# Kernel optimization log

Hardware: AMD Instinct MI355X
Metric: run time of the kernel (lower is better)

## Reference

```python
import jax, jax.numpy as jnp
import numpy as np

B, N, L, H = 8, 64, 256, 768
E = 2 * H            # 1536, concat(subj, obj)
NH = 12              # attention heads
HD = E // NH         # 128 head dim
HL = 1024            # LSTM hidden
C = 42               # num classes
SCALE = 0.02         # param scale for numerical sanity


def setup_inputs() -> dict:
    key = jax.random.key(0)
    ks = jax.random.split(key, 19)
    rn = lambda k, s: jax.random.normal(k, s, jnp.float32) * SCALE
    return {
        "hidden": jax.random.normal(ks[0], (B, N, L, H), jnp.float32),
        "entity_pair_inds": jax.random.randint(ks[1], (B, N, 2), 0, L),
        "Wkey": jax.random.uniform(ks[2], (E, E), jnp.float32) * SCALE,
        "Wque": jax.random.uniform(ks[3], (E, E), jnp.float32) * SCALE,
        "Wval": jax.random.uniform(ks[4], (E, E), jnp.float32) * SCALE,
        "in_proj_w": rn(ks[5], (3 * E, E)),
        "in_proj_b": rn(ks[6], (3 * E,)),
        "out_proj_w": rn(ks[7], (E, E)),
        "out_proj_b": rn(ks[8], (E,)),
        "Wih_f": rn(ks[9], (4 * HL, E)),
        "Whh_f": rn(ks[10], (4 * HL, HL)),
        "bih_f": rn(ks[11], (4 * HL,)),
        "bhh_f": rn(ks[12], (4 * HL,)),
        "Wih_b": rn(ks[13], (4 * HL, E)),
        "Whh_b": rn(ks[14], (4 * HL, HL)),
        "bih_b": rn(ks[15], (4 * HL,)),
        "bhh_b": rn(ks[16], (4 * HL,)),
        "out_w": rn(ks[17], (C, 2 * HL)),
        "out_b": rn(ks[18], (C,)),
    }


def _mha(q_in, k_in, v_in, in_proj_w, in_proj_b, out_proj_w, out_proj_b):
    # torch nn.MultiheadAttention, batch_first
    Wq, Wk, Wv = jnp.split(in_proj_w, 3, axis=0)
    bq, bk, bv = jnp.split(in_proj_b, 3, axis=0)
    b, n, _ = q_in.shape
    q = (q_in @ Wq.T + bq).reshape(b, n, NH, HD)
    k = (k_in @ Wk.T + bk).reshape(b, n, NH, HD)
    v = (v_in @ Wv.T + bv).reshape(b, n, NH, HD)
    scores = jnp.einsum("bnhd,bmhd->bhnm", q, k) / np.sqrt(HD).astype(np.float32)
    attn = jax.nn.softmax(scores, axis=-1)
    o = jnp.einsum("bhnm,bmhd->bnhd", attn, v).reshape(b, n, E)
    return o @ out_proj_w.T + out_proj_b


def _lstm_dir(x, Wih, Whh, bih, bhh):
    # single-direction LSTM over an unbatched sequence x: (T, E)
    def step(carry, xt):
        h, c = carry
        g = xt @ Wih.T + bih + h @ Whh.T + bhh  # (4*HL,)
        i, f, gg, o = jnp.split(g, 4)
        i, f, o = jax.nn.sigmoid(i), jax.nn.sigmoid(f), jax.nn.sigmoid(o)
        c = f * c + i * jnp.tanh(gg)
        h = o * jnp.tanh(c)
        return (h, c), h
    init = (jnp.zeros(HL, x.dtype), jnp.zeros(HL, x.dtype))
    _, hs = jax.lax.scan(step, init, x)
    return hs  # (T, HL)


def reference(hidden, entity_pair_inds, Wkey, Wque, Wval, in_proj_w, in_proj_b,
              out_proj_w, out_proj_b, Wih_f, Whh_f, bih_f, bhh_f,
              Wih_b, Whh_b, bih_b, bhh_b, out_w, out_b):
    # vectorized entity-pair gather: (B, N, 2) indices into token axis L
    idx = entity_pair_inds[:, :, :, None]                      # (B,N,2,1)
    pair = jnp.take_along_axis(hidden, idx, axis=2)            # (B,N,2,H)
    cat = pair.reshape(B, N, 2 * H)                            # (B,N,1536) = [subj; obj]
    keys = cat @ Wkey
    queries = cat @ Wque
    values = cat @ Wval
    # original calls attn(keys, queries, values) -> query=keys, key=queries, value=values
    attn_out = _mha(keys, queries, values, in_proj_w, in_proj_b, out_proj_w, out_proj_b)
    avg = jnp.sum(attn_out * cat, axis=1) / N                  # (B, E)
    # dropout is identity in eval mode
    # torch LSTM treats 2D input as unbatched sequence of length B
    hf = _lstm_dir(avg, Wih_f, Whh_f, bih_f, bhh_f)            # (B, HL)
    hb = _lstm_dir(avg[::-1], Wih_b, Whh_b, bih_b, bhh_b)[::-1]
    lstm_out = jnp.concatenate([hf, hb], axis=-1)              # (B, 2*HL)
    logits = lstm_out @ out_w.T + out_b                        # (B, C)
    return jax.nn.softmax(logits, axis=1)
```

## Files before the change

kernel.cpp:

```cpp
#include <hip/hip_runtime.h>
#include <hip/hip_bf16.h>
#include <cstdint>


typedef __attribute__((ext_vector_type(8))) short short8_t;
typedef __attribute__((ext_vector_type(4))) float f32x4_t;

__device__ __forceinline__ uint4 pack8(float4 a, float4 b) {
  union { uint4 u; __hip_bfloat16 h[8]; } pk;
  pk.h[0] = __float2bfloat16(a.x); pk.h[1] = __float2bfloat16(a.y);
  pk.h[2] = __float2bfloat16(a.z); pk.h[3] = __float2bfloat16(a.w);
  pk.h[4] = __float2bfloat16(b.x); pk.h[5] = __float2bfloat16(b.y);
  pk.h[6] = __float2bfloat16(b.z); pk.h[7] = __float2bfloat16(b.w);
  return pk.u;
}

__global__ __launch_bounds__(256) void prep_all_kernel(
    const float* __restrict__ hidden, const int* __restrict__ inds,
    const float* __restrict__ Wkey, const float* __restrict__ Wque, const float* __restrict__ Wval,
    const float* __restrict__ Whh_f, const float* __restrict__ Whh_b,
    float* __restrict__ cat, __hip_bfloat16* __restrict__ cat16,
    __hip_bfloat16* __restrict__ Wt16, __hip_bfloat16* __restrict__ whh16s,
    float* __restrict__ avg0) {
  const int bid = blockIdx.x, tid = threadIdx.x;
  if (bid < 512) {
    if (bid < 48) avg0[bid * 256 + tid] = 0.f;
    int bn = bid;
    int i0 = inds[bn * 2 + 0], i1 = inds[bn * 2 + 1];
    const float* r0 = hidden + ((size_t)bn * 256 + i0) * 768;
    const float* r1 = hidden + ((size_t)bn * 256 + i1) * 768;
    float* c = cat + (size_t)bn * 1536;
    __hip_bfloat16* c16 = cat16 + (size_t)bn * 1536;
    for (int i = tid; i < 768; i += 256) {
      float a = r0[i], b = r1[i];
      c[i] = a; c[768 + i] = b;
      c16[i] = __float2bfloat16(a); c16[768 + i] = __float2bfloat16(b);
    }
  } else if (bid < 7424) {
    int b2 = bid - 512;
    int z = b2 / 2304, rem = b2 % 2304, by = rem / 48, bx = rem % 48;
    const float* W = z == 0 ? Wkey : (z == 1 ? Wque : Wval);
    __hip_bfloat16* O = Wt16 + (size_t)z * 1536 * 1536;
    __shared__ float tile[32][33];
    int n0 = bx * 32, k0 = by * 32;
    int r = tid >> 3, c4 = (tid & 7) * 4;
    float4 v = *(const float4*)(W + (size_t)(k0 + r) * 1536 + n0 + c4);
    tile[r][c4] = v.x; tile[r][c4 + 1] = v.y; tile[r][c4 + 2] = v.z; tile[r][c4 + 3] = v.w;
    __syncthreads();
    union { ushort4 u; __hip_bfloat16 h[4]; } pk;
#pragma unroll
    for (int j = 0; j < 4; ++j) pk.h[j] = __float2bfloat16(tile[c4 + j][r]);
    *(ushort4*)(O + (size_t)(n0 + r) * 1536 + k0 + c4) = pk.u;
  } else {
    int id = (bid - 7424) * 256 + tid;
    int lane = id & 63, half = (id >> 6) & 1, row = (id >> 7) & 4095, d = id >> 19;
    const float* W = d ? Whh_b : Whh_f;
    const float* srcp = W + (size_t)row * 1024 + half * 512 + lane;
    union { uint4 u; __hip_bfloat16 h[8]; } pk;
#pragma unroll
    for (int e = 0; e < 8; ++e) pk.h[e] = __float2bfloat16(srcp[e * 64]);
    *(uint4*)(whh16s + (size_t)id * 8) = pk.u;
  }
}

template <int CMODE, bool BIAS, bool BF32B>
__global__ __launch_bounds__(256) void mfma_gemm(
    const __hip_bfloat16* __restrict__ A, long As,
    const void* __restrict__ Bmv, long Bs,
    const float* __restrict__ bias, long biasS,
    void* __restrict__ Cp, long Cs,
    const float* __restrict__ catp, float* __restrict__ avgp) {
  constexpr int K = 1536, N = 1536;
  const int z = blockIdx.z;
  A += (size_t)z * As;
  if (BIAS) bias += (size_t)z * biasS;
  __shared__ __align__(16) short Abuf[64 * 64];
  __shared__ __align__(16) short Bbuf[64 * 64];
  const int t = threadIdx.x;
  const int i0 = blockIdx.y * 64, j0 = blockIdx.x * 64;
  const int row = t >> 2, kq = t & 3;
  const int lane = t & 63, wave = t >> 6, wr = wave >> 1, wc = wave & 1;
  f32x4_t acc[2][2] = {};

  const char* Ag = (const char*)(A + (size_t)(i0 + row) * K) + kq * 32;
  const char* Bg;
  if (BF32B)
    Bg = (const char*)((const float*)Bmv + (size_t)z * Bs + (size_t)(j0 + row) * K) + kq * 64;
  else
    Bg = (const char*)((const __hip_bfloat16*)Bmv + (size_t)z * Bs + (size_t)(j0 + row) * K) + kq * 32;
  const int swz = (row & 7) << 4;
  char* Asw0 = (char*)Abuf + ((row * 128 + kq * 32) ^ swz);
  char* Asw1 = (char*)Abuf + ((row * 128 + kq * 32 + 16) ^ swz);
  char* Bsw0 = (char*)Bbuf + ((row * 128 + kq * 32) ^ swz);
  char* Bsw1 = (char*)Bbuf + ((row * 128 + kq * 32 + 16) ^ swz);

  for (int kb = 0; kb < K * 2; kb += 128) {
    uint4 a0 = *(const uint4*)(Ag + kb);
    uint4 a1 = *(const uint4*)(Ag + kb + 16);
    uint4 b0, b1;
    if (BF32B) {
      const char* p = Bg + kb * 2;
      float4 f0 = *(const float4*)(p);
      float4 f1 = *(const float4*)(p + 16);
      float4 f2 = *(const float4*)(p + 32);
      float4 f3 = *(const float4*)(p + 48);
      b0 = pack8(f0, f1); b1 = pack8(f2, f3);
    } else {
      b0 = *(const uint4*)(Bg + kb);
      b1 = *(const uint4*)(Bg + kb + 16);
    }
    __syncthreads();
    *(uint4*)Asw0 = a0; *(uint4*)Asw1 = a1;
    *(uint4*)Bsw0 = b0; *(uint4*)Bsw1 = b1;
    __syncthreads();
#pragma unroll
    for (int ks = 0; ks < 2; ++ks) {
      short8_t af[2], bfr[2];
#pragma unroll
      for (int mi = 0; mi < 2; ++mi) {
        int rr = wr * 32 + mi * 16 + (lane & 15);
        int off = (rr * 128 + ks * 64 + (lane >> 4) * 16) ^ ((rr & 7) << 4);
        af[mi] = *(const short8_t*)((const char*)Abuf + off);
      }
#pragma unroll
      for (int ni = 0; ni < 2; ++ni) {
        int rr = wc * 32 + ni * 16 + (lane & 15);
        int off = (rr * 128 + ks * 64 + (lane >> 4) * 16) ^ ((rr & 7) << 4);
        bfr[ni] = *(const short8_t*)((const char*)Bbuf + off);
      }
#pragma unroll
      for (int mi = 0; mi < 2; ++mi)
#pragma unroll
        for (int ni = 0; ni < 2; ++ni)
          acc[mi][ni] = __builtin_amdgcn_mfma_f32_16x16x32_bf16(af[mi], bfr[ni], acc[mi][ni], 0, 0, 0);
    }
  }
  if (CMODE == 2) {
#pragma unroll
    for (int ni = 0; ni < 2; ++ni) {
      int col = j0 + wc * 32 + ni * 16 + (lane & 15);
      float bv = bias[col];
      float p = 0.f;
#pragma unroll
      for (int mi = 0; mi < 2; ++mi) {
        int rbase = i0 + wr * 32 + mi * 16 + (lane >> 4) * 4;
#pragma unroll
        for (int r = 0; r < 4; ++r) {
          float val = acc[mi][ni][r] + bv;
          p += val * catp[(size_t)(rbase + r) * 1536 + col];
        }
      }
      p += __shfl_xor(p, 16);
      p += __shfl_xor(p, 32);
      if (lane < 16) atomicAdd(&avgp[(size_t)blockIdx.y * 1536 + col], p * (1.0f / 64.0f));
    }
  } else {
#pragma unroll
    for (int mi = 0; mi < 2; ++mi)
#pragma unroll
      for (int ni = 0; ni < 2; ++ni) {
        int r0 = i0 + wr * 32 + mi * 16 + (lane >> 4) * 4;
        int col = j0 + wc * 32 + ni * 16 + (lane & 15);
        float bv = BIAS ? bias[col] : 0.f;
#pragma unroll
        for (int r = 0; r < 4; ++r) {
          float val = acc[mi][ni][r] + bv;
          if (CMODE == 1)
            ((__hip_bfloat16*)Cp)[(size_t)z * Cs + (size_t)(r0 + r) * N + col] = __float2bfloat16(val);
          else
            ((float*)Cp)[(size_t)z * Cs + (size_t)(r0 + r) * N + col] = val;
        }
      }
  }
}

__global__ __launch_bounds__(256) void attn2_kernel(
    const __hip_bfloat16* __restrict__ qkv, __hip_bfloat16* __restrict__ o) {
  __shared__ __align__(16) ushort Qs[64 * 128];
  __shared__ __align__(16) ushort Ks[64 * 128];
  __shared__ __align__(16) ushort Vt[128 * 72];
  __shared__ __align__(16) ushort Ps[64 * 72];
  __shared__ float redmax[2][64];
  __shared__ float redsum[2][64];
  const int b = blockIdx.x / 12, h = blockIdx.x % 12;
  const int tid = threadIdx.x, lane = tid & 63, wave = tid >> 6;
  const int wr = wave >> 1, wc = wave & 1;
  const size_t base = (size_t)b * 64 * 1536 + (size_t)h * 128;
  const __hip_bfloat16* qg = qkv + base;
  const __hip_bfloat16* kg = qkv + 786432 + base;
  const __hip_bfloat16* vg = qkv + 2 * 786432 + base;

  for (int s = tid; s < 1024; s += 256) {
    int row = s >> 4, q4 = s & 15;
    int q4s = (q4 & 8) | ((q4 & 7) ^ (row & 7));
    uint4 qv = *(const uint4*)(qg + (size_t)row * 1536 + q4 * 8);
    uint4 kv = *(const uint4*)(kg + (size_t)row * 1536 + q4 * 8);
    *(uint4*)&Qs[row * 128 + q4s * 8] = qv;
    *(uint4*)&Ks[row * 128 + q4s * 8] = kv;
    uint4 vv = *(const uint4*)(vg + (size_t)row * 1536 + q4 * 8);
    const ushort* ve = (const ushort*)&vv;
    int colv = (((row >> 3) ^ (q4 & 7)) << 3) | (row & 7);
#pragma unroll
    for (int e = 0; e < 8; ++e) Vt[(q4 * 8 + e) * 72 + colv] = ve[e];
  }
  __syncthreads();

  f32x4_t sacc[2][2] = {};
#pragma unroll
  for (int ks = 0; ks < 4; ++ks) {
    short8_t qf[2], kf[2];
#pragma unroll
    for (int mi = 0; mi < 2; ++mi) {
      int rr = wr * 32 + mi * 16 + (lane & 15);
      int slot = ks * 4 + (lane >> 4);
      int slot2 = (slot & 8) | ((slot & 7) ^ (rr & 7));
      qf[mi] = *(const short8_t*)&Qs[rr * 128 + slot2 * 8];
    }
#pragma unroll
    for (int ni = 0; ni < 2; ++ni) {
      int rr = wc * 32 + ni * 16 + (lane & 15);
      int slot = ks * 4 + (lane >> 4);
      int slot2 = (slot & 8) | ((slot & 7) ^ (rr & 7));
      kf[ni] = *(const short8_t*)&Ks[rr * 128 + slot2 * 8];
    }
#pragma unroll
    for (int mi = 0; mi < 2; ++mi)
#pragma unroll
      for (int ni = 0; ni < 2; ++ni)
        sacc[mi][ni] = __builtin_amdgcn_mfma_f32_16x16x32_bf16(qf[mi], kf[ni], sacc[mi][ni], 0, 0, 0);
  }

  const float scale = 0.08838834764831845f;
  float pv[2][2][4];
#pragma unroll
  for (int mi = 0; mi < 2; ++mi)
#pragma unroll
    for (int r = 0; r < 4; ++r) {
      float a0 = sacc[mi][0][r] * scale, a1 = sacc[mi][1][r] * scale;
      pv[mi][0][r] = a0; pv[mi][1][r] = a1;
      float m0 = fmaxf(a0, a1);
      m0 = fmaxf(m0, __shfl_xor(m0, 1));
      m0 = fmaxf(m0, __shfl_xor(m0, 2));
      m0 = fmaxf(m0, __shfl_xor(m0, 4));
      m0 = fmaxf(m0, __shfl_xor(m0, 8));
      if ((lane & 15) == 0) redmax[wc][wr * 32 + mi * 16 + (lane >> 4) * 4 + r] = m0;
    }
  __syncthreads();
#pragma unroll
  for (int mi = 0; mi < 2; ++mi)
#pragma unroll
    for (int r = 0; r < 4; ++r) {
      int row = wr * 32 + mi * 16 + (lane >> 4) * 4 + r;
      float gm = fmaxf(redmax[0][row], redmax[1][row]);
      float e0 = __expf(pv[mi][0][r] - gm);
      float e1 = __expf(pv[mi][1][r] - gm);
      pv[mi][0][r] = e0; pv[mi][1][r] = e1;
      float s0 = e0 + e1;
      s0 += __shfl_xor(s0, 1);
      s0 += __shfl_xor(s0, 2);
      s0 += __shfl_xor(s0, 4);
      s0 += __shfl_xor(s0, 8);
      if ((lane & 15) == 0) redsum[wc][row] = s0;
      int col0 = wc * 32 + (lane & 15);
      Ps[row * 72 + col0] = __bfloat16_as_ushort(__float2bfloat16(e0));
      Ps[row * 72 + col0 + 16] = __bfloat16_as_ushort(__float2bfloat16(e1));
    }
  __syncthreads();

  f32x4_t oacc[2][4] = {};
#pragma unroll
  for (int ks = 0; ks < 2; ++ks) {
    short8_t pf[2], vf[4];
#pragma unroll
    for (int mi = 0; mi < 2; ++mi) {
      int rr = wr * 32 + mi * 16 + (lane & 15);
      pf[mi] = *(const short8_t*)&Ps[rr * 72 + ks * 32 + (lane >> 4) * 8];
    }
#pragma unroll
    for (int ni = 0; ni < 4; ++ni) {
      int rr = wc * 64 + ni * 16 + (lane & 15);
      int mb = (ks * 4 + (lane >> 4)) ^ ((rr >> 3) & 7);
      vf[ni] = *(const short8_t*)&Vt[rr * 72 + mb * 8];
    }
#pragma unroll
    for (int mi = 0; mi < 2; ++mi)
#pragma unroll
      for (int ni = 0; ni < 4; ++ni)
        oacc[mi][ni] = __builtin_amdgcn_mfma_f32_16x16x32_bf16(pf[mi], vf[ni], oacc[mi][ni], 0, 0, 0);
  }

#pragma unroll
  for (int mi = 0; mi < 2; ++mi)
#pragma unroll
    for (int r = 0; r < 4; ++r) {
      int row = wr * 32 + mi * 16 + (lane >> 4) * 4 + r;
      float inv = 1.f / (redsum[0][row] + redsum[1][row]);
#pragma unroll
      for (int ni = 0; ni < 4; ++ni) {
        int col = wc * 64 + ni * 16 + (lane & 15);
        o[base + (size_t)row * 1536 + col] = __float2bfloat16(oacc[mi][ni][r] * inv);
      }
    }
}

__global__ __launch_bounds__(256) void lstm_pre2_kernel(
    const float* __restrict__ avg,
    const float* __restrict__ Wih_f, const float* __restrict__ bih_f, const float* __restrict__ bhh_f,
    const float* __restrict__ Wih_b, const float* __restrict__ bih_b, const float* __restrict__ bhh_b,
    float* __restrict__ xg) {
  int g = blockIdx.x * 4 + (threadIdx.x >> 6);
  int lane = threadIdx.x & 63;
  int d = g >> 12, j = g & 4095;
  const float* W = d ? Wih_b : Wih_f;
  const float4* wrow = (const float4*)(W + (size_t)j * 1536);
  float4 w[6];
#pragma unroll
  for (int c = 0; c < 6; ++c) w[c] = wrow[c * 64 + lane];
  float s[8] = {};
#pragma unroll
  for (int r = 0; r < 8; ++r) {
    const float4* av = (const float4*)(avg + (size_t)r * 1536);
#pragma unroll
    for (int c = 0; c < 6; ++c) {
      float4 x = av[c * 64 + lane];
      s[r] += w[c].x * x.x + w[c].y * x.y + w[c].z * x.z + w[c].w * x.w;
    }
  }
#pragma unroll
  for (int r = 0; r < 8; ++r)
#pragma unroll
    for (int off = 32; off; off >>= 1) s[r] += __shfl_xor(s[r], off);
  if (lane == 0) {
    float bias = d ? (bih_b[j] + bhh_b[j]) : (bih_f[j] + bhh_f[j]);
#pragma unroll
    for (int r = 0; r < 8; ++r) xg[((size_t)d * 8 + r) * 4096 + j] = s[r] + bias;
  }
}

__global__ __launch_bounds__(256) void lstm_step2_kernel(
    const __hip_bfloat16* __restrict__ whh16s, const float* __restrict__ xg,
    float* __restrict__ hstate, float* __restrict__ cstate,
    float* __restrict__ hout, int s) {
  const int bid = blockIdx.x;
  const int d = bid >> 8, u0 = (bid & 255) * 4;
  const int tid = threadIdx.x, wave = tid >> 6, lane = tid & 63;
  const float* hread = hstate + ((size_t)(s & 1) * 2 + d) * 1024;
  float* hwrite = hstate + ((size_t)((s + 1) & 1) * 2 + d) * 1024;
  float* c = cstate + (size_t)d * 1024;
  const int r = d ? (7 - s) : s;

  float hreg[16];
  if (s == 0) {
#pragma unroll
    for (int cc = 0; cc < 16; ++cc) hreg[cc] = 0.f;
  } else {
#pragma unroll
    for (int cc = 0; cc < 16; ++cc) hreg[cc] = hread[cc * 64 + lane];
  }

  __shared__ float gsm[4][4];
#pragma unroll
  for (int ui = 0; ui < 4; ++ui) {
    int row = wave * 1024 + u0 + ui;
    const uint4* wp = (const uint4*)whh16s + ((size_t)d * 4096 + row) * 128 + lane;
    uint4 w0 = wp[0];
    uint4 w1 = wp[64];
    float sacc = 0.f;
#pragma unroll
    for (int e4 = 0; e4 < 4; ++e4) {
      uint32_t u = ((const uint32_t*)&w0)[e4];
      sacc += __uint_as_float(u << 16) * hreg[2 * e4] +
              __uint_as_float(u & 0xffff0000u) * hreg[2 * e4 + 1];
    }
#pragma unroll
    for (int e4 = 0; e4 < 4; ++e4) {
      uint32_t u = ((const uint32_t*)&w1)[e4];
      sacc += __uint_as_float(u << 16) * hreg[8 + 2 * e4] +
              __uint_as_float(u & 0xffff0000u) * hreg[8 + 2 * e4 + 1];
    }
#pragma unroll
    for (int off = 32; off; off >>= 1) sacc += __shfl_xor(sacc, off);
    if (lane == 0) gsm[wave][ui] = sacc;
  }
  __syncthreads();
  if (tid < 4) {
    int u = u0 + tid;
    const float* xgr = xg + ((size_t)d * 8 + r) * 4096;
    float gi = gsm[0][tid] + xgr[u];
    float gf = gsm[1][tid] + xgr[1024 + u];
    float gg = gsm[2][tid] + xgr[2048 + u];
    float go = gsm[3][tid] + xgr[3072 + u];
    float iv = 1.f / (1.f + __expf(-gi));
    float fv = 1.f / (1.f + __expf(-gf));
    float ov = 1.f / (1.f + __expf(-go));
    float cold = (s == 0) ? 0.f : c[u];
    float cn = fv * cold + iv * tanhf(gg);
    float hn = ov * tanhf(cn);
    c[u] = cn;
    hwrite[u] = hn;
    hout[((size_t)d * 8 + r) * 1024 + u] = hn;
  }
}

__global__ __launch_bounds__(256) void final_kernel(
    const float* __restrict__ hout, const float* __restrict__ out_w,
    const float* __restrict__ out_b, float* __restrict__ outp) {
  __shared__ float lo[2048];
  __shared__ float logits[64];
  const int s = blockIdx.x, tid = threadIdx.x;
  for (int i = tid; i < 1024; i += 256) {
    lo[i] = hout[(size_t)s * 1024 + i];
    lo[1024 + i] = hout[(size_t)(8 + s) * 1024 + i];
  }
  __syncthreads();
  const int wave = tid >> 6, lane = tid & 63;
  for (int cls = wave; cls < 42; cls += 4) {
    const float4* wr = (const float4*)(out_w + (size_t)cls * 2048);
    const float4* xr = (const float4*)lo;
    float acc = 0.f;
#pragma unroll
    for (int t = 0; t < 8; ++t) {
      int k4 = lane + t * 64;
      float4 w = wr[k4];
      float4 x = xr[k4];
      acc += w.x * x.x + w.y * x.y + w.z * x.z + w.w * x.w;
    }
#pragma unroll
    for (int off = 32; off; off >>= 1) acc += __shfl_xor(acc, off);
    if (lane == 0) logits[cls] = acc + out_b[cls];
  }
  __syncthreads();
  if (tid == 0) {
    float mx = -1e30f;
    for (int c2 = 0; c2 < 42; ++c2) mx = fmaxf(mx, logits[c2]);
    float sum = 0.f;
    for (int c2 = 0; c2 < 42; ++c2) {
      float e = __expf(logits[c2] - mx);
      logits[c2] = e;
      sum += e;
    }
    float inv = 1.f / sum;
    for (int c2 = 0; c2 < 42; ++c2) outp[s * 42 + c2] = logits[c2] * inv;
  }
}

extern "C" void kernel_launch(void* const* d_in, const int* in_sizes, int n_in,
                              void* d_out, int out_size, void* d_ws, size_t ws_size,
                              hipStream_t stream) {
  const float* hidden     = (const float*)d_in[0];
  const int*   inds       = (const int*)d_in[1];
  const float* Wkey       = (const float*)d_in[2];
  const float* Wque       = (const float*)d_in[3];
  const float* Wval       = (const float*)d_in[4];
  const float* in_proj_w  = (const float*)d_in[5];
  const float* in_proj_b  = (const float*)d_in[6];
  const float* out_proj_w = (const float*)d_in[7];
  const float* out_proj_b = (const float*)d_in[8];
  const float* Wih_f      = (const float*)d_in[9];
  const float* Whh_f      = (const float*)d_in[10];
  const float* bih_f      = (const float*)d_in[11];
  const float* bhh_f      = (const float*)d_in[12];
  const float* Wih_b      = (const float*)d_in[13];
  const float* Whh_b      = (const float*)d_in[14];
  const float* bih_b      = (const float*)d_in[15];
  const float* bhh_b      = (const float*)d_in[16];
  const float* out_w      = (const float*)d_in[17];
  const float* out_b      = (const float*)d_in[18];
  float* out = (float*)d_out;

  float* ws = (float*)d_ws;
  float* cat      = ws;
  float* avg      = cat + 786432;
  float* xg       = avg + 12288;
  float* hstate   = xg + 65536;
  float* cstate   = hstate + 4096;
  float* hout     = cstate + 2048;
  __hip_bfloat16* b16 = (__hip_bfloat16*)(hout + 16384);
  __hip_bfloat16* cat16  = b16;
  __hip_bfloat16* Wt16   = cat16 + 786432;
  __hip_bfloat16* kqv1   = Wt16 + 7077888;
  __hip_bfloat16* qkv16  = kqv1 + 2359296;
  __hip_bfloat16* ob16   = qkv16 + 2359296;
  __hip_bfloat16* whh16s = ob16 + 786432;

  prep_all_kernel<<<11520, 256, 0, stream>>>(hidden, inds, Wkey, Wque, Wval, Whh_f, Whh_b,
                                             cat, cat16, Wt16, whh16s, avg);

  mfma_gemm<1, false, false><<<dim3(24, 8, 3), 256, 0, stream>>>(
      cat16, 0, Wt16, 1536L * 1536, nullptr, 0, kqv1, 786432, nullptr, nullptr);
  mfma_gemm<1, true, true><<<dim3(24, 8, 3), 256, 0, stream>>>(
      kqv1, 786432, in_proj_w, 1536L * 1536, in_proj_b, 1536, qkv16, 786432, nullptr, nullptr);

  attn2_kernel<<<96, 256, 0, stream>>>(qkv16, ob16);

  mfma_gemm<2, true, true><<<dim3(24, 8, 1), 256, 0, stream>>>(
      ob16, 0, out_proj_w, 0, out_proj_b, 0, nullptr, 0, cat, avg);

  lstm_pre2_kernel<<<2048, 256, 0, stream>>>(avg, Wih_f, bih_f, bhh_f, Wih_b, bih_b, bhh_b, xg);

  for (int s = 0; s < 8; ++s)
    lstm_step2_kernel<<<512, 256, 0, stream>>>(whh16s, xg, hstate, cstate, hout, s);

  final_kernel<<<8, 256, 0, stream>>>(hout, out_w, out_b, out);
}
```

Baseline: 164.0 us.

## Fuse first LSTM step into input-projection kernel and remap GEMM block order

The LSTM input-projection kernel now groups the four gate rows for one hidden unit in a block. At step 0, where h and c are zero, it computes that unit's cell and hidden state directly, so one step-kernel launch is removed. The step kernel loses its s==0 special case and always reads the state written by the new kernel. The GEMM kernels also remap their block index so that consecutive blocks are grouped into 8-wide column strips, meant to improve L2 locality. The atomic-add row index is updated to match the new mapping.

```diff
diff --git a/kernel.cpp b/kernel.cpp
--- a/kernel.cpp
+++ b/kernel.cpp
@@ -77,7 +77,10 @@
   __shared__ __align__(16) short Abuf[64 * 64];
   __shared__ __align__(16) short Bbuf[64 * 64];
   const int t = threadIdx.x;
-  const int i0 = blockIdx.y * 64, j0 = blockIdx.x * 64;
+  const int L = blockIdx.y * 24 + blockIdx.x;
+  const int bxs = (L & 7) + 8 * ((L >> 3) % 3);
+  const int bys = (L >> 3) / 3;
+  const int i0 = bys * 64, j0 = bxs * 64;
   const int row = t >> 2, kq = t & 3;
   const int lane = t & 63, wave = t >> 6, wr = wave >> 1, wc = wave & 1;
   f32x4_t acc[2][2] = {};
@@ -152,7 +155,7 @@
       }
       p += __shfl_xor(p, 16);
       p += __shfl_xor(p, 32);
-      if (lane < 16) atomicAdd(&avgp[(size_t)blockIdx.y * 1536 + col], p * (1.0f / 64.0f));
+      if (lane < 16) atomicAdd(&avgp[(size_t)bys * 1536 + col], p * (1.0f / 64.0f));
     }
   } else {
 #pragma unroll
@@ -303,14 +306,17 @@
     }
 }
 
-__global__ __launch_bounds__(256) void lstm_pre2_kernel(
+__global__ __launch_bounds__(256) void lstm_pre3_kernel(
     const float* __restrict__ avg,
     const float* __restrict__ Wih_f, const float* __restrict__ bih_f, const float* __restrict__ bhh_f,
     const float* __restrict__ Wih_b, const float* __restrict__ bih_b, const float* __restrict__ bhh_b,
-    float* __restrict__ xg) {
-  int g = blockIdx.x * 4 + (threadIdx.x >> 6);
-  int lane = threadIdx.x & 63;
-  int d = g >> 12, j = g & 4095;
+    float* __restrict__ xg, float* __restrict__ hstate, float* __restrict__ cstate,
+    float* __restrict__ hout) {
+  __shared__ float g4[4];
+  const int bid = blockIdx.x, tid = threadIdx.x;
+  const int wave = tid >> 6, lane = tid & 63;
+  const int d = bid >> 10, u = bid & 1023;
+  const int j = wave * 1024 + u;
   const float* W = d ? Wih_b : Wih_f;
   const float4* wrow = (const float4*)(W + (size_t)j * 1536);
   float4 w[6];
@@ -330,10 +336,22 @@
   for (int r = 0; r < 8; ++r)
 #pragma unroll
     for (int off = 32; off; off >>= 1) s[r] += __shfl_xor(s[r], off);
+  const int r0 = d ? 7 : 0;
   if (lane == 0) {
     float bias = d ? (bih_b[j] + bhh_b[j]) : (bih_f[j] + bhh_f[j]);
 #pragma unroll
     for (int r = 0; r < 8; ++r) xg[((size_t)d * 8 + r) * 4096 + j] = s[r] + bias;
+    g4[wave] = s[r0] + bias;
+  }
+  __syncthreads();
+  if (tid == 0) {
+    float iv = 1.f / (1.f + __expf(-g4[0]));
+    float ov = 1.f / (1.f + __expf(-g4[3]));
+    float cn = iv * tanhf(g4[2]);
+    float hn = ov * tanhf(cn);
+    cstate[(size_t)d * 1024 + u] = cn;
+    hstate[(size_t)(2 + d) * 1024 + u] = hn;
+    hout[((size_t)d * 8 + r0) * 1024 + u] = hn;
   }
 }
 
@@ -350,13 +368,8 @@
   const int r = d ? (7 - s) : s;
 
   float hreg[16];
-  if (s == 0) {
-#pragma unroll
-    for (int cc = 0; cc < 16; ++cc) hreg[cc] = 0.f;
-  } else {
-#pragma unroll
-    for (int cc = 0; cc < 16; ++cc) hreg[cc] = hread[cc * 64 + lane];
-  }
+#pragma unroll
+  for (int cc = 0; cc < 16; ++cc) hreg[cc] = hread[cc * 64 + lane];
 
   __shared__ float gsm[4][4];
 #pragma unroll
@@ -393,7 +406,7 @@
     float iv = 1.f / (1.f + __expf(-gi));
     float fv = 1.f / (1.f + __expf(-gf));
     float ov = 1.f / (1.f + __expf(-go));
-    float cold = (s == 0) ? 0.f : c[u];
+    float cold = c[u];
     float cn = fv * cold + iv * tanhf(gg);
     float hn = ov * tanhf(cn);
     c[u] = cn;
@@ -496,9 +509,10 @@
   mfma_gemm<2, true, true><<<dim3(24, 8, 1), 256, 0, stream>>>(
       ob16, 0, out_proj_w, 0, out_proj_b, 0, nullptr, 0, cat, avg);
 
-  lstm_pre2_kernel<<<2048, 256, 0, stream>>>(avg, Wih_f, bih_f, bhh_f, Wih_b, bih_b, bhh_b, xg);
-
-  for (int s = 0; s < 8; ++s)
+  lstm_pre3_kernel<<<2048, 256, 0, stream>>>(avg, Wih_f, bih_f, bhh_f, Wih_b, bih_b, bhh_b,
+                                             xg, hstate, cstate, hout);
+
+  for (int s = 1; s < 8; ++s)
     lstm_step2_kernel<<<512, 256, 0, stream>>>(whh16s, xg, hstate, cstate, hout, s);
 
   final_kernel<<<8, 256, 0, stream>>>(hout, out_w, out_b, out);
```

Measured after the change: 159.3 us. 1.03x faster.
